# Optimization experiments

Hardware: AMD Instinct MI355X
Metric: run time of the kernel (lower is better)

The kernel has to match this reference:

```python
import jax, jax.numpy as jnp
import numpy as np

B, NH, T, N, D = 4, 8, 2048, 512, 128
THETA = 2.0 ** 16
GAMMA = 0.995


def setup_inputs() -> dict:
    key = jax.random.key(0)
    kq, kv, ks = jax.random.split(key, 3)
    Q = jax.random.normal(kq, (B, NH, T, N), jnp.float32)
    V = jax.random.normal(kv, (B, NH, T, D), jnp.float32)
    S_prev = 0.01 * jax.random.normal(ks, (B, NH, N, D), jnp.float32)
    # get_freqs(N, theta=2**16): per-channel inverse frequencies
    freqs = jnp.asarray(1.0 / THETA ** (np.arange(N, dtype=np.float32) / N), jnp.float32)
    gamma = jnp.float32(GAMMA)
    return {"Q": Q, "V": V, "S_prev": S_prev, "freqs": freqs, "gamma": gamma}


def _rope(phases, v):
    """Rotary embedding with per-channel phases. phases broadcasts against v's
    last two dims (T, N); rotate-half formulation."""
    cos, sin = jnp.cos(phases), jnp.sin(phases)
    half = v.shape[-1] // 2
    v_rot = jnp.concatenate([-v[..., half:], v[..., :half]], axis=-1)
    return v * cos + v_rot * sin


def reference(Q, V, S_prev, freqs, gamma):
    # Q: (B,nh,T,N)  V: (B,nh,T,D)  S_prev: (B,nh,N,D)
    t_len = Q.shape[2]
    phases = jnp.arange(t_len, dtype=freqs.dtype)[:, None] * freqs[None, :]  # (T,N)
    QR = _rope(phases[None, None], Q)  # K == Q per the module's assert

    q_seq = jnp.moveaxis(QR, 2, 0)  # (T,B,nh,N)
    v_seq = jnp.moveaxis(V, 2, 0)   # (T,B,nh,D)

    def step(S, qv):
        q_t, v_t = qv
        out_t = jnp.einsum('bhn,bhnd->bhd', q_t, S)          # read before write
        S_new = (S + jnp.einsum('bhn,bhd->bhnd', q_t, v_t)) * gamma  # write + decay
        return S_new, out_t

    S_final, outs = jax.lax.scan(step, S_prev, (q_seq, v_seq))
    output = jnp.moveaxis(outs, 0, 2)  # (B,nh,T,D)
    return output, S_final
```

## Files before the change

kernel.cpp:

```cpp
#include <hip/hip_runtime.h>
#include <hip/hip_bf16.h>

typedef __attribute__((ext_vector_type(8))) short short8;
typedef __attribute__((ext_vector_type(4))) float f32x4;

#define MFMA16(a,b,c) __builtin_amdgcn_mfma_f32_16x16x32_bf16((a),(b),(c),0,0,0)

constexpr int BHn = 32;
constexpr int Tn  = 2048;
constexpr int Nn  = 512;
constexpr int Dn  = 128;
constexpr int CHn = 64;
constexpr int NCH = Tn / CHn;

static __device__ __forceinline__ unsigned short f2b(float x){
  __hip_bfloat16 h = __float2bfloat16(x);
  return *reinterpret_cast<unsigned short*>(&h);
}

__global__ __launch_bounds__(256) void rope_k(const float* __restrict__ Q,
                                              const float* __restrict__ freqs,
                                              unsigned short* __restrict__ QR){
  int gid = blockIdx.x * 256 + threadIdx.x;
  int np  = gid & 255;
  int t   = gid >> 8;
  float tf = (float)t;
  float f1 = freqs[np], f2 = freqs[np + 256];
  float s1, c1, s2, c2;
  sincosf(tf * f1, &s1, &c1);
  sincosf(tf * f2, &s2, &c2);
  size_t off = (size_t)t * Nn + np;
  for (int bh = 0; bh < BHn; ++bh){
    size_t base = (size_t)bh * Tn * Nn + off;
    float q1 = Q[base], q2 = Q[base + 256];
    QR[base]       = f2b(q1 * c1 - q2 * s1);
    QR[base + 256] = f2b(q2 * c2 + q1 * s2);
  }
}

__device__ __forceinline__ short8 ldfrag(const unsigned short* buf, int rowbase, int k0, int ld, int lane){
  int row = rowbase + (lane & 15);
  int col = (k0 + ((lane >> 4) << 3)) ^ ((row & 7) << 3);
  return *reinterpret_cast<const short8*>(buf + row * ld + col);
}
__device__ __forceinline__ short8 ldfragT(const unsigned short* buf, int rowbase, int k0, int lane){
  int row = rowbase + (lane & 15);
  int sw = ((row & 7) ^ ((row >> 3) & 7)) << 3;
  int col = (k0 + ((lane >> 4) << 3)) ^ sw;
  return *reinterpret_cast<const short8*>(buf + row * 64 + col);
}

__global__ __launch_bounds__(512, 1) void lattn_main(
    const unsigned short* __restrict__ QR,
    const float* __restrict__ V,
    const float* __restrict__ S_prev,
    const float* __restrict__ gammap,
    float* __restrict__ Out,
    float* __restrict__ Sfin)
{
  __shared__ __align__(16) unsigned short Rs [64 * 512];
  __shared__ __align__(16) unsigned short RTs[512 * 64];
  __shared__ __align__(16) unsigned short SbTs[16 * 512];
  __shared__ __align__(16) unsigned short VTs[16 * 64];
  __shared__ __align__(16) unsigned short Ps [64 * 64];
  __shared__ float gpow[65], gpinv[65];

  const int tid  = threadIdx.x;
  const int w    = tid >> 6;
  const int lane = tid & 63;
  const int bh   = blockIdx.x & 31;
  const int dch  = blockIdx.x >> 5;
  const int d0   = dch * 16;
  const float g  = gammap[0];

  if (tid < 65){
    gpow[tid]  = powf(g,  (float)tid);
    gpinv[tid] = powf(g, -(float)tid);
  }
  #pragma unroll
  for (int i = tid; i < 64 * 64; i += 512) Ps[i] = 0;

  f32x4 st[8];
  if (w >= 4){
    int r0 = (w - 4) * 8;
    #pragma unroll
    for (int j = 0; j < 8; ++j){
      int n = (r0 + j) * 16 + (lane & 15);
      const float* sp = S_prev + (size_t)bh * Nn * Dn + (size_t)n * Dn + d0 + ((lane >> 4) << 2);
      st[j] = *reinterpret_cast<const f32x4*>(sp);
    }
  }
  __syncthreads();
  const float g64 = gpow[64];

  for (int c = 0; c < NCH; ++c){
    const int t0 = c * CHn;

    if (w >= 4){
      int r0 = (w - 4) * 8;
      #pragma unroll
      for (int j = 0; j < 8; ++j){
        int n  = (r0 + j) * 16 + (lane & 15);
        int dl = ((lane >> 4) << 2);
        #pragma unroll
        for (int r = 0; r < 4; ++r){
          int d = dl + r;
          SbTs[d * 512 + (n ^ ((d & 7) << 3))] = f2b(st[j][r]);
        }
      }
    }
    #pragma unroll
    for (int i = 0; i < 4; ++i){
      int p  = tid + i * 512;
      int dt = (p >> 6) << 1;
      int n0 = (p & 63) << 3;
      const unsigned short* src = QR + (size_t)bh * Tn * Nn + (size_t)(t0 + dt) * Nn + n0;
      uint4 a = *reinterpret_cast<const uint4*>(src);
      uint4 b = *reinterpret_cast<const uint4*>(src + Nn);
      *reinterpret_cast<uint4*>(&Rs[ dt      * 512 + (n0 ^ (( dt      & 7) << 3))]) = a;
      *reinterpret_cast<uint4*>(&Rs[(dt + 1) * 512 + (n0 ^ (((dt + 1) & 7) << 3))]) = b;
      unsigned int aw[4] = {a.x, a.y, a.z, a.w};
      unsigned int bw[4] = {b.x, b.y, b.z, b.w};
      #pragma unroll
      for (int e = 0; e < 8; ++e){
        int n = n0 + e;
        unsigned int lo = (e & 1) ? (aw[e >> 1] >> 16) : (aw[e >> 1] & 0xffffu);
        unsigned int hi = (e & 1) ? (bw[e >> 1] >> 16) : (bw[e >> 1] & 0xffffu);
        int sw = ((n & 7) ^ ((n >> 3) & 7)) << 3;
        *reinterpret_cast<unsigned int*>(&RTs[n * 64 + (dt ^ sw)]) = lo | (hi << 16);
      }
    }
    {
      int dtv = tid >> 3;
      int dp  = (tid & 7) << 1;
      const float* vp = V + (size_t)bh * Tn * Dn + (size_t)(t0 + dtv) * Dn + d0 + dp;
      float sc = gpinv[dtv];
      VTs[ dp      * 64 + (dtv ^ (( dp      & 7) << 3))] = f2b(vp[0] * sc);
      VTs[(dp + 1) * 64 + (dtv ^ (((dp + 1) & 7) << 3))] = f2b(vp[1] * sc);
    }
    __syncthreads();

    f32x4 oacc = {0.f, 0.f, 0.f, 0.f};
    if (w < 4){
      f32x4 p0 = {0.f,0.f,0.f,0.f}, p1 = p0, p2 = p0;
      for (int kb = 0; kb < 16; ++kb){
        int k0 = kb * 32;
        short8 fs = ldfrag(SbTs, 0, k0, 512, lane);
        if (w == 0){
          short8 f0 = ldfrag(Rs,  0, k0, 512, lane);
          short8 f1 = ldfrag(Rs, 16, k0, 512, lane);
          p0   = MFMA16(f0, f0, p0);
          p1   = MFMA16(f1, f0, p1);
          p2   = MFMA16(f1, f1, p2);
          oacc = MFMA16(fs, f0, oacc);
        } else if (w == 1){
          short8 f0 = ldfrag(Rs,  0, k0, 512, lane);
          short8 f1 = ldfrag(Rs, 16, k0, 512, lane);
          short8 f2 = ldfrag(Rs, 32, k0, 512, lane);
          p0   = MFMA16(f2, f0, p0);
          p1   = MFMA16(f2, f1, p1);
          p2   = MFMA16(f2, f2, p2);
          oacc = MFMA16(fs, f2, oacc);
        } else if (w == 2){
          short8 f0 = ldfrag(Rs,  0, k0, 512, lane);
          short8 f1 = ldfrag(Rs, 16, k0, 512, lane);
          short8 f3 = ldfrag(Rs, 48, k0, 512, lane);
          p0   = MFMA16(f3, f0, p0);
          p1   = MFMA16(f3, f1, p1);
          oacc = MFMA16(fs, f3, oacc);
        } else {
          short8 f1 = ldfrag(Rs, 16, k0, 512, lane);
          short8 f2 = ldfrag(Rs, 32, k0, 512, lane);
          short8 f3 = ldfrag(Rs, 48, k0, 512, lane);
          p0   = MFMA16(f3, f2, p0);
          p1   = MFMA16(f3, f3, p1);
          oacc = MFMA16(fs, f1, oacc);
        }
      }
      int tI[3], tJ[3], nt;
      if      (w == 0){ tI[0]=0; tJ[0]=0; tI[1]=1; tJ[1]=0; tI[2]=1; tJ[2]=1; nt = 3; }
      else if (w == 1){ tI[0]=2; tJ[0]=0; tI[1]=2; tJ[1]=1; tI[2]=2; tJ[2]=2; nt = 3; }
      else if (w == 2){ tI[0]=3; tJ[0]=0; tI[1]=3; tJ[1]=1; tI[2]=0; tJ[2]=0; nt = 2; }
      else            { tI[0]=3; tJ[0]=2; tI[1]=3; tJ[1]=3; tI[2]=0; tJ[2]=0; nt = 2; }
      f32x4 pacc[3] = {p0, p1, p2};
      for (int q = 0; q < nt; ++q){
        int j  = tJ[q] * 16 + (lane & 15);
        int i0 = tI[q] * 16 + ((lane >> 4) << 2);
        #pragma unroll
        for (int r = 0; r < 4; ++r){
          int i = i0 + r;
          float v = (j < i) ? pacc[q][r] * gpow[i] : 0.f;
          Ps[i * 64 + (j ^ ((i & 7) << 3))] = f2b(v);
        }
      }
    } else {
      int r0 = (w - 4) * 8;
      #pragma unroll
      for (int ks = 0; ks < 2; ++ks){
        short8 av = ldfrag(VTs, 0, ks * 32, 64, lane);
        #pragma unroll
        for (int j = 0; j < 8; ++j){
          short8 bn = ldfragT(RTs, (r0 + j) * 16, ks * 32, lane);
          st[j] = MFMA16(av, bn, st[j]);
        }
      }
      #pragma unroll
      for (int j = 0; j < 8; ++j)
        #pragma unroll
        for (int r = 0; r < 4; ++r) st[j][r] *= g64;
    }
    __syncthreads();

    if (w < 4){
      const int itl = (w == 0) ? 0 : (w == 1) ? 2 : (w == 2) ? 3 : 1;
      float gi = gpow[itl * 16 + (lane & 15)];
      #pragma unroll
      for (int r = 0; r < 4; ++r) oacc[r] *= gi;
      #pragma unroll
      for (int ks = 0; ks < 2; ++ks){
        short8 av = ldfrag(VTs, 0, ks * 32, 64, lane);
        short8 bp = ldfrag(Ps, itl * 16, ks * 32, 64, lane);
        oacc = MFMA16(av, bp, oacc);
      }
      int ti = t0 + itl * 16 + (lane & 15);
      float* op = Out + (size_t)bh * Tn * Dn + (size_t)ti * Dn + d0 + ((lane >> 4) << 2);
      *reinterpret_cast<f32x4*>(op) = oacc;
    }
    __syncthreads();
  }

  if (w >= 4){
    int r0 = (w - 4) * 8;
    #pragma unroll
    for (int j = 0; j < 8; ++j){
      int n = (r0 + j) * 16 + (lane & 15);
      float* sp = Sfin + (size_t)bh * Nn * Dn + (size_t)n * Dn + d0 + ((lane >> 4) << 2);
      *reinterpret_cast<f32x4*>(sp) = st[j];
    }
  }
}

extern "C" void kernel_launch(void* const* d_in, const int* in_sizes, int n_in,
                              void* d_out, int out_size, void* d_ws, size_t ws_size,
                              hipStream_t stream){
  const float* Q      = (const float*)d_in[0];
  const float* V      = (const float*)d_in[1];
  const float* S_prev = (const float*)d_in[2];
  const float* freqs  = (const float*)d_in[3];
  const float* gamma  = (const float*)d_in[4];
  float* Out  = (float*)d_out;
  float* Sfin = Out + (size_t)BHn * Tn * Dn;
  unsigned short* QR = (unsigned short*)d_ws;

  rope_k<<<2048, 256, 0, stream>>>(Q, freqs, QR);
  lattn_main<<<256, 512, 0, stream>>>(QR, V, S_prev, gamma, Out, Sfin);
}
```

Before: 232.6 us.

## Double block size to 16 waves and prefetch next chunk during compute

```diff
diff --git a/kernel.cpp b/kernel.cpp
--- a/kernel.cpp
+++ b/kernel.cpp
@@ -50,7 +50,23 @@
   return *reinterpret_cast<const short8*>(buf + row * 64 + col);
 }
 
-__global__ __launch_bounds__(512, 1) void lattn_main(
+__device__ __forceinline__ void stage_R(unsigned short* Rs, unsigned short* RTs,
+                                        uint4 a, uint4 b, int dt, int n0){
+  *reinterpret_cast<uint4*>(&Rs[ dt      * 512 + (n0 ^ (( dt      & 7) << 3))]) = a;
+  *reinterpret_cast<uint4*>(&Rs[(dt + 1) * 512 + (n0 ^ (((dt + 1) & 7) << 3))]) = b;
+  unsigned int aw[4] = {a.x, a.y, a.z, a.w};
+  unsigned int bw[4] = {b.x, b.y, b.z, b.w};
+  #pragma unroll
+  for (int e = 0; e < 8; ++e){
+    int n = n0 + e;
+    unsigned int lo = (e & 1) ? (aw[e >> 1] >> 16) : (aw[e >> 1] & 0xffffu);
+    unsigned int hi = (e & 1) ? (bw[e >> 1] >> 16) : (bw[e >> 1] & 0xffffu);
+    int sw = ((n & 7) ^ ((n >> 3) & 7)) << 3;
+    *reinterpret_cast<unsigned int*>(&RTs[n * 64 + (dt ^ sw)]) = lo | (hi << 16);
+  }
+}
+
+__global__ __launch_bounds__(1024, 1) void lattn_main(
     const unsigned short* __restrict__ QR,
     const float* __restrict__ V,
     const float* __restrict__ S_prev,
@@ -61,7 +77,7 @@
   __shared__ __align__(16) unsigned short Rs [64 * 512];
   __shared__ __align__(16) unsigned short RTs[512 * 64];
   __shared__ __align__(16) unsigned short SbTs[16 * 512];
-  __shared__ __align__(16) unsigned short VTs[16 * 64];
+  __shared__ __align__(16) unsigned short VTs[2][16 * 64];
   __shared__ __align__(16) unsigned short Ps [64 * 64];
   __shared__ float gpow[65], gpinv[65];
 
@@ -72,20 +88,22 @@
   const int dch  = blockIdx.x >> 5;
   const int d0   = dch * 16;
   const float g  = gammap[0];
+  const int sidx = w - 8;
+
+  const unsigned short* QRbh = QR + (size_t)bh * Tn * Nn;
+  const float* Vbh = V + (size_t)bh * Tn * Dn;
 
   if (tid < 65){
     gpow[tid]  = powf(g,  (float)tid);
     gpinv[tid] = powf(g, -(float)tid);
   }
-  #pragma unroll
-  for (int i = tid; i < 64 * 64; i += 512) Ps[i] = 0;
-
-  f32x4 st[8];
-  if (w >= 4){
-    int r0 = (w - 4) * 8;
+  for (int i = tid; i < 64 * 64; i += 1024) Ps[i] = 0;
+
+  f32x4 st[4];
+  if (w >= 8){
     #pragma unroll
-    for (int j = 0; j < 8; ++j){
-      int n = (r0 + j) * 16 + (lane & 15);
+    for (int j = 0; j < 4; ++j){
+      int n = (sidx * 4 + j) * 16 + (lane & 15);
       const float* sp = S_prev + (size_t)bh * Nn * Dn + (size_t)n * Dn + d0 + ((lane >> 4) << 2);
       st[j] = *reinterpret_cast<const f32x4*>(sp);
     }
@@ -93,15 +111,28 @@
   __syncthreads();
   const float g64 = gpow[64];
 
-  for (int c = 0; c < NCH; ++c){
-    const int t0 = c * CHn;
-
-    if (w >= 4){
-      int r0 = (w - 4) * 8;
+  {
+    #pragma unroll
+    for (int i = 0; i < 2; ++i){
+      int p  = tid + i * 1024;
+      int dt = (p >> 6) << 1;
+      int n0 = (p & 63) << 3;
+      const unsigned short* src = QRbh + (size_t)dt * Nn + n0;
+      uint4 a = *reinterpret_cast<const uint4*>(src);
+      uint4 b = *reinterpret_cast<const uint4*>(src + Nn);
+      stage_R(Rs, RTs, a, b, dt, n0);
+    }
+    if (w < 8){
+      int dtv = tid >> 3, dp = (tid & 7) << 1;
+      const float* vp = Vbh + (size_t)dtv * Dn + d0 + dp;
+      float sc = gpinv[dtv];
+      VTs[0][ dp      * 64 + (dtv ^ (( dp      & 7) << 3))] = f2b(vp[0] * sc);
+      VTs[0][(dp + 1) * 64 + (dtv ^ (((dp + 1) & 7) << 3))] = f2b(vp[1] * sc);
+    } else {
       #pragma unroll
-      for (int j = 0; j < 8; ++j){
-        int n  = (r0 + j) * 16 + (lane & 15);
-        int dl = ((lane >> 4) << 2);
+      for (int j = 0; j < 4; ++j){
+        int n  = (sidx * 4 + j) * 16 + (lane & 15);
+        int dl = (lane >> 4) << 2;
         #pragma unroll
         for (int r = 0; r < 4; ++r){
           int d = dl + r;
@@ -109,131 +140,166 @@
         }
       }
     }
-    #pragma unroll
-    for (int i = 0; i < 4; ++i){
-      int p  = tid + i * 512;
-      int dt = (p >> 6) << 1;
-      int n0 = (p & 63) << 3;
-      const unsigned short* src = QR + (size_t)bh * Tn * Nn + (size_t)(t0 + dt) * Nn + n0;
-      uint4 a = *reinterpret_cast<const uint4*>(src);
-      uint4 b = *reinterpret_cast<const uint4*>(src + Nn);
-      *reinterpret_cast<uint4*>(&Rs[ dt      * 512 + (n0 ^ (( dt      & 7) << 3))]) = a;
-      *reinterpret_cast<uint4*>(&Rs[(dt + 1) * 512 + (n0 ^ (((dt + 1) & 7) << 3))]) = b;
-      unsigned int aw[4] = {a.x, a.y, a.z, a.w};
-      unsigned int bw[4] = {b.x, b.y, b.z, b.w};
-      #pragma unroll
-      for (int e = 0; e < 8; ++e){
-        int n = n0 + e;
-        unsigned int lo = (e & 1) ? (aw[e >> 1] >> 16) : (aw[e >> 1] & 0xffffu);
-        unsigned int hi = (e & 1) ? (bw[e >> 1] >> 16) : (bw[e >> 1] & 0xffffu);
-        int sw = ((n & 7) ^ ((n >> 3) & 7)) << 3;
-        *reinterpret_cast<unsigned int*>(&RTs[n * 64 + (dt ^ sw)]) = lo | (hi << 16);
-      }
-    }
-    {
-      int dtv = tid >> 3;
-      int dp  = (tid & 7) << 1;
-      const float* vp = V + (size_t)bh * Tn * Dn + (size_t)(t0 + dtv) * Dn + d0 + dp;
-      float sc = gpinv[dtv];
-      VTs[ dp      * 64 + (dtv ^ (( dp      & 7) << 3))] = f2b(vp[0] * sc);
-      VTs[(dp + 1) * 64 + (dtv ^ (((dp + 1) & 7) << 3))] = f2b(vp[1] * sc);
-    }
-    __syncthreads();
-
-    f32x4 oacc = {0.f, 0.f, 0.f, 0.f};
-    if (w < 4){
-      f32x4 p0 = {0.f,0.f,0.f,0.f}, p1 = p0, p2 = p0;
-      for (int kb = 0; kb < 16; ++kb){
-        int k0 = kb * 32;
-        short8 fs = ldfrag(SbTs, 0, k0, 512, lane);
-        if (w == 0){
+  }
+  __syncthreads();
+
+  for (int c = 0; c < NCH; ++c){
+    const int t0 = c * CHn;
+    const int vb = c & 1;
+    const bool pf = (c + 1 < NCH);
+
+    uint4 ra0, rb0, ra1, rb1;
+    float va0 = 0.f, va1 = 0.f;
+    const int dt0_ = (tid >> 6) << 1,          n00_ = (tid & 63) << 3;
+    const int dt1_ = ((tid + 1024) >> 6) << 1, n01_ = n00_;
+    const int dtv_ = tid >> 3;
+    if (pf){
+      const unsigned short* QRc = QRbh + (size_t)(t0 + CHn) * Nn;
+      const unsigned short* s0 = QRc + (size_t)dt0_ * Nn + n00_;
+      ra0 = *reinterpret_cast<const uint4*>(s0);
+      rb0 = *reinterpret_cast<const uint4*>(s0 + Nn);
+      const unsigned short* s1 = QRc + (size_t)dt1_ * Nn + n01_;
+      ra1 = *reinterpret_cast<const uint4*>(s1);
+      rb1 = *reinterpret_cast<const uint4*>(s1 + Nn);
+      if (w < 8){
+        const float* vp = Vbh + (size_t)(t0 + CHn + dtv_) * Dn + d0 + ((tid & 7) << 1);
+        va0 = vp[0]; va1 = vp[1];
+      }
+    }
+
+    f32x4 acc0 = {0.f, 0.f, 0.f, 0.f}, acc1 = acc0;
+    if (w < 8){
+      if (w == 0){
+        for (int kb = 0; kb < 16; ++kb){ int k0 = kb * 32;
           short8 f0 = ldfrag(Rs,  0, k0, 512, lane);
           short8 f1 = ldfrag(Rs, 16, k0, 512, lane);
-          p0   = MFMA16(f0, f0, p0);
-          p1   = MFMA16(f1, f0, p1);
-          p2   = MFMA16(f1, f1, p2);
-          oacc = MFMA16(fs, f0, oacc);
-        } else if (w == 1){
+          acc0 = MFMA16(f0, f0, acc0);
+          acc1 = MFMA16(f1, f0, acc1); }
+      } else if (w == 1){
+        for (int kb = 0; kb < 16; ++kb){ int k0 = kb * 32;
           short8 f0 = ldfrag(Rs,  0, k0, 512, lane);
           short8 f1 = ldfrag(Rs, 16, k0, 512, lane);
           short8 f2 = ldfrag(Rs, 32, k0, 512, lane);
-          p0   = MFMA16(f2, f0, p0);
-          p1   = MFMA16(f2, f1, p1);
-          p2   = MFMA16(f2, f2, p2);
-          oacc = MFMA16(fs, f2, oacc);
-        } else if (w == 2){
+          acc0 = MFMA16(f1, f1, acc0);
+          acc1 = MFMA16(f2, f0, acc1); }
+      } else if (w == 2){
+        for (int kb = 0; kb < 16; ++kb){ int k0 = kb * 32;
+          short8 f1 = ldfrag(Rs, 16, k0, 512, lane);
+          short8 f2 = ldfrag(Rs, 32, k0, 512, lane);
+          acc0 = MFMA16(f2, f1, acc0);
+          acc1 = MFMA16(f2, f2, acc1); }
+      } else if (w == 3){
+        for (int kb = 0; kb < 16; ++kb){ int k0 = kb * 32;
           short8 f0 = ldfrag(Rs,  0, k0, 512, lane);
           short8 f1 = ldfrag(Rs, 16, k0, 512, lane);
           short8 f3 = ldfrag(Rs, 48, k0, 512, lane);
-          p0   = MFMA16(f3, f0, p0);
-          p1   = MFMA16(f3, f1, p1);
-          oacc = MFMA16(fs, f3, oacc);
-        } else {
-          short8 f1 = ldfrag(Rs, 16, k0, 512, lane);
+          acc0 = MFMA16(f3, f0, acc0);
+          acc1 = MFMA16(f3, f1, acc1); }
+      } else if (w == 4){
+        for (int kb = 0; kb < 16; ++kb){ int k0 = kb * 32;
           short8 f2 = ldfrag(Rs, 32, k0, 512, lane);
           short8 f3 = ldfrag(Rs, 48, k0, 512, lane);
-          p0   = MFMA16(f3, f2, p0);
-          p1   = MFMA16(f3, f3, p1);
-          oacc = MFMA16(fs, f1, oacc);
-        }
-      }
-      int tI[3], tJ[3], nt;
-      if      (w == 0){ tI[0]=0; tJ[0]=0; tI[1]=1; tJ[1]=0; tI[2]=1; tJ[2]=1; nt = 3; }
-      else if (w == 1){ tI[0]=2; tJ[0]=0; tI[1]=2; tJ[1]=1; tI[2]=2; tJ[2]=2; nt = 3; }
-      else if (w == 2){ tI[0]=3; tJ[0]=0; tI[1]=3; tJ[1]=1; tI[2]=0; tJ[2]=0; nt = 2; }
-      else            { tI[0]=3; tJ[0]=2; tI[1]=3; tJ[1]=3; tI[2]=0; tJ[2]=0; nt = 2; }
-      f32x4 pacc[3] = {p0, p1, p2};
-      for (int q = 0; q < nt; ++q){
-        int j  = tJ[q] * 16 + (lane & 15);
-        int i0 = tI[q] * 16 + ((lane >> 4) << 2);
-        #pragma unroll
-        for (int r = 0; r < 4; ++r){
-          int i = i0 + r;
-          float v = (j < i) ? pacc[q][r] * gpow[i] : 0.f;
-          Ps[i * 64 + (j ^ ((i & 7) << 3))] = f2b(v);
-        }
+          acc0 = MFMA16(f3, f2, acc0);
+          acc1 = MFMA16(f3, f3, acc1); }
+      } else if (w == 5){
+        for (int kb = 0; kb < 16; ++kb){ int k0 = kb * 32;
+          short8 fs = ldfrag(SbTs, 0, k0, 512, lane);
+          short8 f0 = ldfrag(Rs,  0, k0, 512, lane);
+          short8 f1 = ldfrag(Rs, 16, k0, 512, lane);
+          acc0 = MFMA16(fs, f0, acc0);
+          acc1 = MFMA16(fs, f1, acc1); }
+      } else if (w == 6){
+        for (int kb = 0; kb < 16; ++kb){ int k0 = kb * 32;
+          short8 fs = ldfrag(SbTs, 0, k0, 512, lane);
+          short8 f2 = ldfrag(Rs, 32, k0, 512, lane);
+          acc0 = MFMA16(fs, f2, acc0); }
+      } else {
+        for (int kb = 0; kb < 16; ++kb){ int k0 = kb * 32;
+          short8 fs = ldfrag(SbTs, 0, k0, 512, lane);
+          short8 f3 = ldfrag(Rs, 48, k0, 512, lane);
+          acc0 = MFMA16(fs, f3, acc0); }
+      }
+      if (w < 5){
+        auto pwrite = [&](f32x4 pa, int tI, int tJ){
+          int j  = tJ * 16 + (lane & 15);
+          int i0 = tI * 16 + ((lane >> 4) << 2);
+          #pragma unroll
+          for (int r = 0; r < 4; ++r){
+            int i = i0 + r;
+            float v = (j < i) ? pa[r] * gpow[i] : 0.f;
+            Ps[i * 64 + (j ^ ((i & 7) << 3))] = f2b(v);
+          }
+        };
+        if      (w == 0){ pwrite(acc0, 0, 0); pwrite(acc1, 1, 0); }
+        else if (w == 1){ pwrite(acc0, 1, 1); pwrite(acc1, 2, 0); }
+        else if (w == 2){ pwrite(acc0, 2, 1); pwrite(acc1, 2, 2); }
+        else if (w == 3){ pwrite(acc0, 3, 0); pwrite(acc1, 3, 1); }
+        else            { pwrite(acc0, 3, 2); pwrite(acc1, 3, 3); }
       }
     } else {
-      int r0 = (w - 4) * 8;
       #pragma unroll
       for (int ks = 0; ks < 2; ++ks){
-        short8 av = ldfrag(VTs, 0, ks * 32, 64, lane);
-        #pragma unroll
-        for (int j = 0; j < 8; ++j){
-          short8 bn = ldfragT(RTs, (r0 + j) * 16, ks * 32, lane);
+        short8 av = ldfrag(VTs[vb], 0, ks * 32, 64, lane);
+        #pragma unroll
+        for (int j = 0; j < 4; ++j){
+          short8 bn = ldfragT(RTs, (sidx * 4 + j) * 16, ks * 32, lane);
           st[j] = MFMA16(av, bn, st[j]);
         }
       }
       #pragma unroll
-      for (int j = 0; j < 8; ++j)
+      for (int j = 0; j < 4; ++j)
         #pragma unroll
         for (int r = 0; r < 4; ++r) st[j][r] *= g64;
     }
     __syncthreads();
 
-    if (w < 4){
-      const int itl = (w == 0) ? 0 : (w == 1) ? 2 : (w == 2) ? 3 : 1;
-      float gi = gpow[itl * 16 + (lane & 15)];
+    if (w >= 8){
       #pragma unroll
-      for (int r = 0; r < 4; ++r) oacc[r] *= gi;
-      #pragma unroll
-      for (int ks = 0; ks < 2; ++ks){
-        short8 av = ldfrag(VTs, 0, ks * 32, 64, lane);
-        short8 bp = ldfrag(Ps, itl * 16, ks * 32, 64, lane);
-        oacc = MFMA16(av, bp, oacc);
-      }
-      int ti = t0 + itl * 16 + (lane & 15);
-      float* op = Out + (size_t)bh * Tn * Dn + (size_t)ti * Dn + d0 + ((lane >> 4) << 2);
-      *reinterpret_cast<f32x4*>(op) = oacc;
+      for (int j = 0; j < 4; ++j){
+        int n  = (sidx * 4 + j) * 16 + (lane & 15);
+        int dl = (lane >> 4) << 2;
+        #pragma unroll
+        for (int r = 0; r < 4; ++r){
+          int d = dl + r;
+          SbTs[d * 512 + (n ^ ((d & 7) << 3))] = f2b(st[j][r]);
+        }
+      }
+    } else if (w >= 5){
+      auto outE = [&](f32x4 o, int itl){
+        float gi = gpow[itl * 16 + (lane & 15)];
+        #pragma unroll
+        for (int r = 0; r < 4; ++r) o[r] *= gi;
+        #pragma unroll
+        for (int ks = 0; ks < 2; ++ks){
+          short8 av = ldfrag(VTs[vb], 0, ks * 32, 64, lane);
+          short8 bp = ldfrag(Ps, itl * 16, ks * 32, 64, lane);
+          o = MFMA16(av, bp, o);
+        }
+        int ti = t0 + itl * 16 + (lane & 15);
+        float* op = Out + (size_t)bh * Tn * Dn + (size_t)ti * Dn + d0 + ((lane >> 4) << 2);
+        *reinterpret_cast<f32x4*>(op) = o;
+      };
+      if      (w == 5){ outE(acc0, 0); outE(acc1, 1); }
+      else if (w == 6){ outE(acc0, 2); }
+      else            { outE(acc0, 3); }
+    }
+    if (pf){
+      stage_R(Rs, RTs, ra0, rb0, dt0_, n00_);
+      stage_R(Rs, RTs, ra1, rb1, dt1_, n01_);
+      if (w < 8){
+        int dp = (tid & 7) << 1;
+        float sc = gpinv[dtv_];
+        VTs[vb ^ 1][ dp      * 64 + (dtv_ ^ (( dp      & 7) << 3))] = f2b(va0 * sc);
+        VTs[vb ^ 1][(dp + 1) * 64 + (dtv_ ^ (((dp + 1) & 7) << 3))] = f2b(va1 * sc);
+      }
     }
     __syncthreads();
   }
 
-  if (w >= 4){
-    int r0 = (w - 4) * 8;
+  if (w >= 8){
     #pragma unroll
-    for (int j = 0; j < 8; ++j){
-      int n = (r0 + j) * 16 + (lane & 15);
+    for (int j = 0; j < 4; ++j){
+      int n = (sidx * 4 + j) * 16 + (lane & 15);
       float* sp = Sfin + (size_t)bh * Nn * Dn + (size_t)n * Dn + d0 + ((lane >> 4) << 2);
       *reinterpret_cast<f32x4*>(sp) = st[j];
     }
@@ -253,5 +319,5 @@
   unsigned short* QR = (unsigned short*)d_ws;
 
   rope_k<<<2048, 256, 0, stream>>>(Q, freqs, QR);
-  lattn_main<<<256, 512, 0, stream>>>(QR, V, S_prev, gamma, Out, Sfin);
-}
+  lattn_main<<<256, 1024, 0, stream>>>(QR, V, S_prev, gamma, Out, Sfin);
+}
```

After: 292.3 us. 1.26x slower.

## Prefetch next chunk's QR and V into registers and overlap staging with compute

Applied to the files above, without the earlier changes.

```diff
diff --git a/kernel.cpp b/kernel.cpp
--- a/kernel.cpp
+++ b/kernel.cpp
@@ -50,6 +50,22 @@
   return *reinterpret_cast<const short8*>(buf + row * 64 + col);
 }
 
+__device__ __forceinline__ void stage_R(unsigned short* Rs, unsigned short* RTs,
+                                        uint4 a, uint4 b, int dt, int n0){
+  *reinterpret_cast<uint4*>(&Rs[ dt      * 512 + (n0 ^ (( dt      & 7) << 3))]) = a;
+  *reinterpret_cast<uint4*>(&Rs[(dt + 1) * 512 + (n0 ^ (((dt + 1) & 7) << 3))]) = b;
+  unsigned int aw[4] = {a.x, a.y, a.z, a.w};
+  unsigned int bw[4] = {b.x, b.y, b.z, b.w};
+  #pragma unroll
+  for (int e = 0; e < 8; ++e){
+    int n = n0 + e;
+    unsigned int lo = (e & 1) ? (aw[e >> 1] >> 16) : (aw[e >> 1] & 0xffffu);
+    unsigned int hi = (e & 1) ? (bw[e >> 1] >> 16) : (bw[e >> 1] & 0xffffu);
+    int sw = ((n & 7) ^ ((n >> 3) & 7)) << 3;
+    *reinterpret_cast<unsigned int*>(&RTs[n * 64 + (dt ^ sw)]) = lo | (hi << 16);
+  }
+}
+
 __global__ __launch_bounds__(512, 1) void lattn_main(
     const unsigned short* __restrict__ QR,
     const float* __restrict__ V,
@@ -61,7 +77,7 @@
   __shared__ __align__(16) unsigned short Rs [64 * 512];
   __shared__ __align__(16) unsigned short RTs[512 * 64];
   __shared__ __align__(16) unsigned short SbTs[16 * 512];
-  __shared__ __align__(16) unsigned short VTs[16 * 64];
+  __shared__ __align__(16) unsigned short VTs[2][16 * 64];
   __shared__ __align__(16) unsigned short Ps [64 * 64];
   __shared__ float gpow[65], gpinv[65];
 
@@ -72,6 +88,9 @@
   const int dch  = blockIdx.x >> 5;
   const int d0   = dch * 16;
   const float g  = gammap[0];
+
+  const unsigned short* QRbh = QR + (size_t)bh * Tn * Nn;
+  const float* Vbh = V + (size_t)bh * Tn * Dn;
 
   if (tid < 65){
     gpow[tid]  = powf(g,  (float)tid);
@@ -93,52 +112,61 @@
   __syncthreads();
   const float g64 = gpow[64];
 
-  for (int c = 0; c < NCH; ++c){
-    const int t0 = c * CHn;
-
-    if (w >= 4){
-      int r0 = (w - 4) * 8;
-      #pragma unroll
-      for (int j = 0; j < 8; ++j){
-        int n  = (r0 + j) * 16 + (lane & 15);
-        int dl = ((lane >> 4) << 2);
-        #pragma unroll
-        for (int r = 0; r < 4; ++r){
-          int d = dl + r;
-          SbTs[d * 512 + (n ^ ((d & 7) << 3))] = f2b(st[j][r]);
-        }
-      }
-    }
+  {
     #pragma unroll
     for (int i = 0; i < 4; ++i){
       int p  = tid + i * 512;
       int dt = (p >> 6) << 1;
       int n0 = (p & 63) << 3;
-      const unsigned short* src = QR + (size_t)bh * Tn * Nn + (size_t)(t0 + dt) * Nn + n0;
+      const unsigned short* src = QRbh + (size_t)dt * Nn + n0;
       uint4 a = *reinterpret_cast<const uint4*>(src);
       uint4 b = *reinterpret_cast<const uint4*>(src + Nn);
-      *reinterpret_cast<uint4*>(&Rs[ dt      * 512 + (n0 ^ (( dt      & 7) << 3))]) = a;
-      *reinterpret_cast<uint4*>(&Rs[(dt + 1) * 512 + (n0 ^ (((dt + 1) & 7) << 3))]) = b;
-      unsigned int aw[4] = {a.x, a.y, a.z, a.w};
-      unsigned int bw[4] = {b.x, b.y, b.z, b.w};
-      #pragma unroll
-      for (int e = 0; e < 8; ++e){
-        int n = n0 + e;
-        unsigned int lo = (e & 1) ? (aw[e >> 1] >> 16) : (aw[e >> 1] & 0xffffu);
-        unsigned int hi = (e & 1) ? (bw[e >> 1] >> 16) : (bw[e >> 1] & 0xffffu);
-        int sw = ((n & 7) ^ ((n >> 3) & 7)) << 3;
-        *reinterpret_cast<unsigned int*>(&RTs[n * 64 + (dt ^ sw)]) = lo | (hi << 16);
-      }
+      stage_R(Rs, RTs, a, b, dt, n0);
     }
     {
-      int dtv = tid >> 3;
-      int dp  = (tid & 7) << 1;
-      const float* vp = V + (size_t)bh * Tn * Dn + (size_t)(t0 + dtv) * Dn + d0 + dp;
+      int dtv = tid >> 3, dp = (tid & 7) << 1;
+      const float* vp = Vbh + (size_t)dtv * Dn + d0 + dp;
       float sc = gpinv[dtv];
-      VTs[ dp      * 64 + (dtv ^ (( dp      & 7) << 3))] = f2b(vp[0] * sc);
-      VTs[(dp + 1) * 64 + (dtv ^ (((dp + 1) & 7) << 3))] = f2b(vp[1] * sc);
-    }
-    __syncthreads();
+      VTs[0][ dp      * 64 + (dtv ^ (( dp      & 7) << 3))] = f2b(vp[0] * sc);
+      VTs[0][(dp + 1) * 64 + (dtv ^ (((dp + 1) & 7) << 3))] = f2b(vp[1] * sc);
+    }
+    if (w >= 4){
+      int r0 = (w - 4) * 8;
+      #pragma unroll
+      for (int j = 0; j < 8; ++j){
+        int n  = (r0 + j) * 16 + (lane & 15);
+        int dl = (lane >> 4) << 2;
+        #pragma unroll
+        for (int r = 0; r < 4; ++r){
+          int d = dl + r;
+          SbTs[d * 512 + (n ^ ((d & 7) << 3))] = f2b(st[j][r]);
+        }
+      }
+    }
+  }
+  __syncthreads();
+
+  for (int c = 0; c < NCH; ++c){
+    const int t0 = c * CHn;
+    const int vb = c & 1;
+    const bool pf = (c + 1 < NCH);
+
+    uint4 ra[4], rb[4];
+    float va0 = 0.f, va1 = 0.f;
+    const int n0_  = (tid & 63) << 3;
+    const int dtv_ = tid >> 3;
+    if (pf){
+      const unsigned short* QRc = QRbh + (size_t)(t0 + CHn) * Nn;
+      #pragma unroll
+      for (int i = 0; i < 4; ++i){
+        int dt = (((tid >> 6) + 8 * i) << 1);
+        const unsigned short* src = QRc + (size_t)dt * Nn + n0_;
+        ra[i] = *reinterpret_cast<const uint4*>(src);
+        rb[i] = *reinterpret_cast<const uint4*>(src + Nn);
+      }
+      const float* vp = Vbh + (size_t)(t0 + CHn + dtv_) * Dn + d0 + ((tid & 7) << 1);
+      va0 = vp[0]; va1 = vp[1];
+    }
 
     f32x4 oacc = {0.f, 0.f, 0.f, 0.f};
     if (w < 4){
@@ -197,7 +225,7 @@
       int r0 = (w - 4) * 8;
       #pragma unroll
       for (int ks = 0; ks < 2; ++ks){
-        short8 av = ldfrag(VTs, 0, ks * 32, 64, lane);
+        short8 av = ldfrag(VTs[vb], 0, ks * 32, 64, lane);
         #pragma unroll
         for (int j = 0; j < 8; ++j){
           short8 bn = ldfragT(RTs, (r0 + j) * 16, ks * 32, lane);
@@ -211,20 +239,43 @@
     }
     __syncthreads();
 
-    if (w < 4){
+    if (w >= 4){
+      int r0 = (w - 4) * 8;
+      #pragma unroll
+      for (int j = 0; j < 8; ++j){
+        int n  = (r0 + j) * 16 + (lane & 15);
+        int dl = (lane >> 4) << 2;
+        #pragma unroll
+        for (int r = 0; r < 4; ++r){
+          int d = dl + r;
+          SbTs[d * 512 + (n ^ ((d & 7) << 3))] = f2b(st[j][r]);
+        }
+      }
+    } else {
       const int itl = (w == 0) ? 0 : (w == 1) ? 2 : (w == 2) ? 3 : 1;
       float gi = gpow[itl * 16 + (lane & 15)];
       #pragma unroll
       for (int r = 0; r < 4; ++r) oacc[r] *= gi;
       #pragma unroll
       for (int ks = 0; ks < 2; ++ks){
-        short8 av = ldfrag(VTs, 0, ks * 32, 64, lane);
+        short8 av = ldfrag(VTs[vb], 0, ks * 32, 64, lane);
         short8 bp = ldfrag(Ps, itl * 16, ks * 32, 64, lane);
         oacc = MFMA16(av, bp, oacc);
       }
       int ti = t0 + itl * 16 + (lane & 15);
       float* op = Out + (size_t)bh * Tn * Dn + (size_t)ti * Dn + d0 + ((lane >> 4) << 2);
       *reinterpret_cast<f32x4*>(op) = oacc;
+    }
+    if (pf){
+      #pragma unroll
+      for (int i = 0; i < 4; ++i){
+        int dt = (((tid >> 6) + 8 * i) << 1);
+        stage_R(Rs, RTs, ra[i], rb[i], dt, n0_);
+      }
+      int dp = (tid & 7) << 1;
+      float sc = gpinv[dtv_];
+      VTs[vb ^ 1][ dp      * 64 + (dtv_ ^ (( dp      & 7) << 3))] = f2b(va0 * sc);
+      VTs[vb ^ 1][(dp + 1) * 64 + (dtv_ ^ (((dp + 1) & 7) << 3))] = f2b(va1 * sc);
     }
     __syncthreads();
   }
```

New measurement: 227.1 us. 2.4% less time.
